# Kernel optimization log

Hardware: AMD Instinct MI355X
Metric: run time of the kernel (lower is better)

## Reference

```python
import jax, jax.numpy as jnp
import numpy as np

OUT_F, IN_F = 16384, 4096
TOKENS = 8192
PALETTE = 256


def setup_inputs() -> dict:
    key = jax.random.key(0)
    k1, k2, k3, k4 = jax.random.split(key, 4)
    input = jax.random.normal(k1, (TOKENS, IN_F), dtype=jnp.float32)
    weight_idx = jax.random.randint(k2, (OUT_F, IN_F), 0, PALETTE, dtype=jnp.int32)
    lookup_table = jax.random.normal(k3, (PALETTE,), dtype=jnp.float32)
    bias = jax.random.normal(k4, (OUT_F,), dtype=jnp.float32)
    return {"input": input, "weight_idx": weight_idx, "lookup_table": lookup_table, "bias": bias}


def reference(input, weight_idx, lookup_table, bias):
    # Dequantize: LUT gather expands uint8 indices to full-precision weights [out, in]
    full_weights = lookup_table[weight_idx]
    # F.linear: y = x @ W^T + b
    return jnp.einsum('ti,oi->to', input, full_weights) + bias
```

## Files before the change

### kernel.cpp

```cpp
#include <hip/hip_runtime.h>
#include <hip/hip_bf16.h>
#include <stdint.h>

#define TOKENS 8192
#define OUT_F  16384
#define IN_F   4096

typedef short bf16x8 __attribute__((ext_vector_type(8)));
typedef float f32x4  __attribute__((ext_vector_type(4)));

__device__ __forceinline__ unsigned short bf16_rne(float f) {
    union { float f; unsigned int u; } v; v.f = f;
    unsigned int u = v.u;
    u += 0x7fffu + ((u >> 16) & 1u);
    return (unsigned short)(u >> 16);
}

__device__ __forceinline__ unsigned int pack_bf16x2(float a, float b) {
    return (unsigned int)bf16_rne(a) | ((unsigned int)bf16_rne(b) << 16);
}

__device__ __forceinline__ void async_cp16(const void* gptr, void* ldsptr) {
    __builtin_amdgcn_global_load_lds(
        (const __attribute__((address_space(1))) unsigned int*)gptr,
        (__attribute__((address_space(3))) unsigned int*)ldsptr,
        16, 0, 0);
}

__global__ __launch_bounds__(256) void cvt_input_kernel(
    const float* __restrict__ in, unsigned short* __restrict__ out, int n8)
{
    int i = blockIdx.x * 256 + threadIdx.x;
    if (i >= n8) return;
    size_t base = (size_t)i * 8;
    float4 a = *(const float4*)(in + base);
    float4 b = *(const float4*)(in + base + 4);
    uint4 p;
    p.x = pack_bf16x2(a.x, a.y);  p.y = pack_bf16x2(a.z, a.w);
    p.z = pack_bf16x2(b.x, b.y);  p.w = pack_bf16x2(b.z, b.w);
    *(uint4*)(out + base) = p;
}

__global__ __launch_bounds__(256) void dequant_kernel(
    const int* __restrict__ idx, const float* __restrict__ lut,
    unsigned short* __restrict__ out, int n8)
{
    __shared__ float slut[256];
    slut[threadIdx.x] = lut[threadIdx.x];
    __syncthreads();
    int i = blockIdx.x * 256 + threadIdx.x;
    if (i >= n8) return;
    size_t base = (size_t)i * 8;
    int4 i0 = *(const int4*)(idx + base);
    int4 i1 = *(const int4*)(idx + base + 4);
    uint4 p;
    p.x = pack_bf16x2(slut[i0.x], slut[i0.y]);
    p.y = pack_bf16x2(slut[i0.z], slut[i0.w]);
    p.z = pack_bf16x2(slut[i1.x], slut[i1.y]);
    p.w = pack_bf16x2(slut[i1.z], slut[i1.w]);
    *(uint4*)(out + base) = p;
}

template<int MODE>
__global__ __launch_bounds__(256) void palett_gemm(
    const unsigned short* __restrict__ A,
    const unsigned short* __restrict__ B,
    const float* __restrict__ Af,
    const int* __restrict__ Widx,
    const float* __restrict__ lut,
    const float* __restrict__ bias,
    float* __restrict__ out)
{
    __shared__ __align__(16) unsigned short smA[128 * 32];
    __shared__ __align__(16) unsigned short smB[128 * 32];
    __shared__ float slut[256];

    const int t    = threadIdx.x;
    const int w    = t >> 6;
    const int l    = t & 63;
    const int quad = l >> 4;
    const int r16  = l & 15;
    const int wr   = w >> 1;
    const int wc   = w & 1;

    const int m0 = blockIdx.y * 128;
    const int n0 = blockIdx.x * 128;

    const int g0  = t * 8;
    const int row = g0 >> 5;
    const int col = g0 & 31;

    char* const smA_c = (char*)smA;
    char* const smB_c = (char*)smB;

    if constexpr (MODE == 1) {
        slut[t] = lut[t];
        __syncthreads();
    }

    uint32_t aoff[4], boff[4];
#pragma unroll
    for (int i = 0; i < 4; ++i) {
        aoff[i] = (uint32_t)(((wr * 64 + i * 16 + r16) * 32 + quad * 8) * 2);
        boff[i] = (uint32_t)(((wc * 64 + i * 16 + r16) * 32 + quad * 8) * 2);
    }

    f32x4 acc[4][4] = {};

    const unsigned short* a0 = nullptr; const unsigned short* a1 = nullptr;
    const unsigned short* b0 = nullptr; const unsigned short* b1 = nullptr;
    const float* af0 = nullptr; const float* af1 = nullptr;
    const int* wi0 = nullptr;   const int* wi1 = nullptr;
    if constexpr (MODE == 0) {
        a0 = A + (size_t)(m0 + row) * IN_F + col;
        a1 = A + (size_t)(m0 + row + 64) * IN_F + col;
        b0 = B + (size_t)(n0 + row) * IN_F + col;
        b1 = B + (size_t)(n0 + row + 64) * IN_F + col;
    } else {
        af0 = Af + (size_t)(m0 + row) * IN_F + col;
        af1 = Af + (size_t)(m0 + row + 64) * IN_F + col;
        wi0 = Widx + (size_t)(n0 + row) * IN_F + col;
        wi1 = Widx + (size_t)(n0 + row + 64) * IN_F + col;
    }

    const uint32_t ldsw0 = (uint32_t)(w * 1024);
    const uint32_t ldsw1 = (uint32_t)(4096 + w * 1024);

    for (int k0 = 0; k0 < IN_F; k0 += 32) {
        if constexpr (MODE == 0) {
            async_cp16(a0 + k0, smA_c + ldsw0);
            async_cp16(a1 + k0, smA_c + ldsw1);
            async_cp16(b0 + k0, smB_c + ldsw0);
            async_cp16(b1 + k0, smB_c + ldsw1);
        } else {
            float4 x0 = *(const float4*)(af0 + k0);
            float4 x1 = *(const float4*)(af0 + k0 + 4);
            uint4 p;
            p.x = pack_bf16x2(x0.x, x0.y); p.y = pack_bf16x2(x0.z, x0.w);
            p.z = pack_bf16x2(x1.x, x1.y); p.w = pack_bf16x2(x1.z, x1.w);
            *(uint4*)(smA_c + t * 16) = p;
            x0 = *(const float4*)(af1 + k0);
            x1 = *(const float4*)(af1 + k0 + 4);
            p.x = pack_bf16x2(x0.x, x0.y); p.y = pack_bf16x2(x0.z, x0.w);
            p.z = pack_bf16x2(x1.x, x1.y); p.w = pack_bf16x2(x1.z, x1.w);
            *(uint4*)(smA_c + 4096 + t * 16) = p;

            int4 j0 = *(const int4*)(wi0 + k0);
            int4 j1 = *(const int4*)(wi0 + k0 + 4);
            p.x = pack_bf16x2(slut[j0.x], slut[j0.y]);
            p.y = pack_bf16x2(slut[j0.z], slut[j0.w]);
            p.z = pack_bf16x2(slut[j1.x], slut[j1.y]);
            p.w = pack_bf16x2(slut[j1.z], slut[j1.w]);
            *(uint4*)(smB_c + t * 16) = p;
            j0 = *(const int4*)(wi1 + k0);
            j1 = *(const int4*)(wi1 + k0 + 4);
            p.x = pack_bf16x2(slut[j0.x], slut[j0.y]);
            p.y = pack_bf16x2(slut[j0.z], slut[j0.w]);
            p.z = pack_bf16x2(slut[j1.x], slut[j1.y]);
            p.w = pack_bf16x2(slut[j1.z], slut[j1.w]);
            *(uint4*)(smB_c + 4096 + t * 16) = p;
        }
        __syncthreads();

        bf16x8 afr[4], bfr[4];
#pragma unroll
        for (int i = 0; i < 4; ++i) afr[i] = *(const bf16x8*)(smA_c + aoff[i]);
#pragma unroll
        for (int j = 0; j < 4; ++j) bfr[j] = *(const bf16x8*)(smB_c + boff[j]);
#pragma unroll
        for (int i = 0; i < 4; ++i)
#pragma unroll
            for (int j = 0; j < 4; ++j)
                acc[i][j] = __builtin_amdgcn_mfma_f32_16x16x32_bf16(
                    afr[i], bfr[j], acc[i][j], 0, 0, 0);
        __syncthreads();
    }

    float bj[4];
#pragma unroll
    for (int j = 0; j < 4; ++j) bj[j] = bias[n0 + wc * 64 + j * 16 + r16];

#pragma unroll
    for (int i = 0; i < 4; ++i) {
        const int mbase = m0 + wr * 64 + i * 16 + quad * 4;
#pragma unroll
        for (int j = 0; j < 4; ++j) {
            const int n = n0 + wc * 64 + j * 16 + r16;
#pragma unroll
            for (int v = 0; v < 4; ++v) {
                out[(size_t)(mbase + v) * OUT_F + n] = acc[i][j][v] + bj[j];
            }
        }
    }
}

extern "C" void kernel_launch(void* const* d_in, const int* in_sizes, int n_in,
                              void* d_out, int out_size, void* d_ws, size_t ws_size,
                              hipStream_t stream) {
    const float* input = (const float*)d_in[0];
    const int*   widx  = (const int*)d_in[1];
    const float* lut   = (const float*)d_in[2];
    const float* bias  = (const float*)d_in[3];
    float* out = (float*)d_out;

    const size_t aBytes = (size_t)TOKENS * IN_F * sizeof(unsigned short);
    const size_t bBytes = (size_t)OUT_F  * IN_F * sizeof(unsigned short);

    dim3 grid(OUT_F / 128, TOKENS / 128);

    if (ws_size >= aBytes + bBytes) {
        unsigned short* wsA = (unsigned short*)d_ws;
        unsigned short* wsB = (unsigned short*)((char*)d_ws + aBytes);
        const int nA8 = (TOKENS * IN_F) / 8;
        const int nB8 = (OUT_F  * IN_F) / 8;
        cvt_input_kernel<<<(nA8 + 255) / 256, 256, 0, stream>>>(input, wsA, nA8);
        dequant_kernel<<<(nB8 + 255) / 256, 256, 0, stream>>>(widx, lut, wsB, nB8);
        palett_gemm<0><<<grid, 256, 0, stream>>>(wsA, wsB, nullptr, nullptr, lut, bias, out);
    } else {
        palett_gemm<1><<<grid, 256, 0, stream>>>(nullptr, nullptr, input, widx, lut, bias, out);
    }
}
```

Baseline: 1.948 ms.

## Replace bf16 GEMM with 256x256 double-buffered, swizzled, interleaved-stage kernel

Replaces the 128x128 single-buffered workspace GEMM with a 512-thread, 256x256-tile kernel. It double-buffers 64-wide K tiles in 128KB of LDS and interleaves async global-to-LDS loads with MFMA quarters under explicit barriers and vmcnt waits. It also XOR-swizzles the LDS columns to avoid bank conflicts, remaps block IDs for L2 locality, and raises wave priority around the MFMAs. The goal is to raise MFMA utilisation by hiding load latency and increasing data reuse per tile. In exchange it brings heavy register pressure and fragile hand-scheduled synchronisation.

```diff
diff --git a/kernel.cpp b/kernel.cpp
--- a/kernel.cpp
+++ b/kernel.cpp
@@ -1,5 +1,4 @@
 #include <hip/hip_runtime.h>
-#include <hip/hip_bf16.h>
 #include <stdint.h>
 
 #define TOKENS 8192
@@ -61,10 +60,154 @@
     *(uint4*)(out + base) = p;
 }
 
-template<int MODE>
-__global__ __launch_bounds__(256) void palett_gemm(
+__global__ __launch_bounds__(512, 2) void palett_gemm256(
     const unsigned short* __restrict__ A,
     const unsigned short* __restrict__ B,
+    const float* __restrict__ bias,
+    float* __restrict__ out)
+{
+    __shared__ __align__(16) char sm[131072];
+
+    const int t    = threadIdx.x;
+    const int w    = t >> 6;
+    const int l    = t & 63;
+    const int quad = l >> 4;
+    const int r16  = l & 15;
+    const int wr   = w >> 2;
+    const int wc   = w & 3;
+
+    const int orig = blockIdx.y * gridDim.x + blockIdx.x;
+    const int swzb = (orig & 7) * 256 + (orig >> 3);
+    const int n0   = (swzb & 63) << 8;
+    const int m0   = (swzb >> 6) << 8;
+
+    const int srow = w * 16 + (l >> 3);
+    const int scol = ((l & 7) ^ (l >> 3)) << 3;
+    const unsigned short* pA = A + (size_t)(m0 + srow) * IN_F + scol;
+    const unsigned short* pB = B + (size_t)(n0 + srow) * IN_F + scol;
+
+    const int cswz  = (r16 & 7) << 4;
+    const int col0  = (quad * 16) ^ cswz;
+    const int col1  = (64 + quad * 16) ^ cswz;
+    const int arow  = r16 * 128;
+    const int abase = wr * 16384;
+    const int bbase = 32768 + (wc >> 1) * 16384 + (wc & 1) * 8192;
+
+    f32x4  acc[8][4] = {};
+    bf16x8 rA[4][2], rB0[2][2], rB1[2][2];
+
+#define BARRIER() asm volatile("s_barrier" ::: "memory")
+
+#define STAGE(P, HOFF, LOFF, KOFF) do {                                          \
+    async_cp16((P) + (size_t)(HOFF) * IN_F + (KOFF), sm + (LOFF) + w * 2048);    \
+    async_cp16((P) + (size_t)((HOFF) + 8) * IN_F + (KOFF),                       \
+               sm + (LOFF) + w * 2048 + 1024);                                   \
+} while (0)
+
+#define READ_A(RB_, MH) do {                                                     \
+    _Pragma("unroll")                                                            \
+    for (int i_ = 0; i_ < 4; ++i_) {                                             \
+        rA[i_][0] = *(const bf16x8*)(sm + (RB_) + abase + ((MH)*4 + i_)*2048 + arow + col0); \
+        rA[i_][1] = *(const bf16x8*)(sm + (RB_) + abase + ((MH)*4 + i_)*2048 + arow + col1); \
+    }                                                                            \
+} while (0)
+
+#define READ_B(DST, RB_, NH) do {                                                \
+    _Pragma("unroll")                                                            \
+    for (int j_ = 0; j_ < 2; ++j_) {                                             \
+        DST[j_][0] = *(const bf16x8*)(sm + (RB_) + bbase + ((NH)*2 + j_)*2048 + arow + col0); \
+        DST[j_][1] = *(const bf16x8*)(sm + (RB_) + bbase + ((NH)*2 + j_)*2048 + arow + col1); \
+    }                                                                            \
+} while (0)
+
+#define MFMA_Q(MH, NH, RB) do {                                                  \
+    _Pragma("unroll")                                                            \
+    for (int i_ = 0; i_ < 4; ++i_) {                                             \
+        _Pragma("unroll")                                                        \
+        for (int j_ = 0; j_ < 2; ++j_) {                                         \
+            acc[(MH)*4+i_][(NH)*2+j_] = __builtin_amdgcn_mfma_f32_16x16x32_bf16( \
+                rA[i_][0], RB[j_][0], acc[(MH)*4+i_][(NH)*2+j_], 0, 0, 0);       \
+            acc[(MH)*4+i_][(NH)*2+j_] = __builtin_amdgcn_mfma_f32_16x16x32_bf16( \
+                rA[i_][1], RB[j_][1], acc[(MH)*4+i_][(NH)*2+j_], 0, 0, 0);       \
+        }                                                                        \
+    }                                                                            \
+} while (0)
+
+#define TILE(RB_, WB_, KOFF) do {                                                \
+                                                \
+    STAGE(pA, 0, (WB_) + 0, KOFF);                                               \
+    asm volatile("s_waitcnt vmcnt(2)" ::: "memory");                             \
+    BARRIER();                                                                   \
+    READ_A(RB_, 0);                                                              \
+    READ_B(rB0, RB_, 0);                                                         \
+    __builtin_amdgcn_s_setprio(1);                                               \
+    MFMA_Q(0, 0, rB0);                                                           \
+    __builtin_amdgcn_s_setprio(0);                                               \
+    READ_B(rB1, RB_, 1);                                                         \
+    BARRIER();                                                                   \
+                            \
+    STAGE(pA, 128, (WB_) + 16384, KOFF);                                         \
+    BARRIER();                                                                   \
+    __builtin_amdgcn_s_setprio(1);                                               \
+    MFMA_Q(0, 1, rB1);                                                           \
+    __builtin_amdgcn_s_setprio(0);                                               \
+    READ_A(RB_, 1);                                                              \
+    BARRIER();                                                                   \
+                                                                    \
+    STAGE(pB, 0, (WB_) + 32768, KOFF);                                           \
+    BARRIER();                                                                   \
+    __builtin_amdgcn_s_setprio(1);                                               \
+    MFMA_Q(1, 0, rB0);                                                           \
+    __builtin_amdgcn_s_setprio(0);                                               \
+    BARRIER();                                                                   \
+                                                                    \
+    STAGE(pB, 128, (WB_) + 49152, KOFF);                                         \
+    BARRIER();                                                                   \
+    __builtin_amdgcn_s_setprio(1);                                               \
+    MFMA_Q(1, 1, rB1);                                                           \
+    __builtin_amdgcn_s_setprio(0);                                               \
+    BARRIER();                                                                   \
+} while (0)
+
+    STAGE(pA, 0,   0,     0);
+    STAGE(pA, 128, 16384, 0);
+    STAGE(pB, 0,   32768, 0);
+    STAGE(pB, 128, 49152, 0);
+
+#pragma unroll 1
+    for (int it = 0; it < 32; ++it) {
+        const int k1 = (2 * it + 1) * 64;
+        const int k2 = ((2 * it + 2) & 63) * 64;
+        TILE(0,     65536, k1);
+        TILE(65536, 0,     k2);
+    }
+    asm volatile("s_waitcnt vmcnt(0)" ::: "memory");
+
+#undef TILE
+#undef MFMA_Q
+#undef READ_B
+#undef READ_A
+#undef STAGE
+#undef BARRIER
+
+    float bj[4];
+#pragma unroll
+    for (int j = 0; j < 4; ++j) bj[j] = bias[n0 + wc * 64 + j * 16 + r16];
+
+#pragma unroll
+    for (int mf = 0; mf < 8; ++mf) {
+        const int mrow = m0 + wr * 128 + mf * 16 + quad * 4;
+#pragma unroll
+        for (int nf = 0; nf < 4; ++nf) {
+            const int n = n0 + wc * 64 + nf * 16 + r16;
+#pragma unroll
+            for (int v = 0; v < 4; ++v)
+                out[(size_t)(mrow + v) * OUT_F + n] = acc[mf][nf][v] + bj[nf];
+        }
+    }
+}
+
+__global__ __launch_bounds__(256) void palett_gemm_fused(
     const float* __restrict__ Af,
     const int* __restrict__ Widx,
     const float* __restrict__ lut,
@@ -93,10 +236,8 @@
     char* const smA_c = (char*)smA;
     char* const smB_c = (char*)smB;
 
-    if constexpr (MODE == 1) {
-        slut[t] = lut[t];
-        __syncthreads();
-    }
+    slut[t] = lut[t];
+    __syncthreads();
 
     uint32_t aoff[4], boff[4];
 #pragma unroll
@@ -107,59 +248,38 @@
 
     f32x4 acc[4][4] = {};
 
-    const unsigned short* a0 = nullptr; const unsigned short* a1 = nullptr;
-    const unsigned short* b0 = nullptr; const unsigned short* b1 = nullptr;
-    const float* af0 = nullptr; const float* af1 = nullptr;
-    const int* wi0 = nullptr;   const int* wi1 = nullptr;
-    if constexpr (MODE == 0) {
-        a0 = A + (size_t)(m0 + row) * IN_F + col;
-        a1 = A + (size_t)(m0 + row + 64) * IN_F + col;
-        b0 = B + (size_t)(n0 + row) * IN_F + col;
-        b1 = B + (size_t)(n0 + row + 64) * IN_F + col;
-    } else {
-        af0 = Af + (size_t)(m0 + row) * IN_F + col;
-        af1 = Af + (size_t)(m0 + row + 64) * IN_F + col;
-        wi0 = Widx + (size_t)(n0 + row) * IN_F + col;
-        wi1 = Widx + (size_t)(n0 + row + 64) * IN_F + col;
-    }
-
-    const uint32_t ldsw0 = (uint32_t)(w * 1024);
-    const uint32_t ldsw1 = (uint32_t)(4096 + w * 1024);
+    const float* af0 = Af + (size_t)(m0 + row) * IN_F + col;
+    const float* af1 = Af + (size_t)(m0 + row + 64) * IN_F + col;
+    const int*   wi0 = Widx + (size_t)(n0 + row) * IN_F + col;
+    const int*   wi1 = Widx + (size_t)(n0 + row + 64) * IN_F + col;
 
     for (int k0 = 0; k0 < IN_F; k0 += 32) {
-        if constexpr (MODE == 0) {
-            async_cp16(a0 + k0, smA_c + ldsw0);
-            async_cp16(a1 + k0, smA_c + ldsw1);
-            async_cp16(b0 + k0, smB_c + ldsw0);
-            async_cp16(b1 + k0, smB_c + ldsw1);
-        } else {
-            float4 x0 = *(const float4*)(af0 + k0);
-            float4 x1 = *(const float4*)(af0 + k0 + 4);
-            uint4 p;
-            p.x = pack_bf16x2(x0.x, x0.y); p.y = pack_bf16x2(x0.z, x0.w);
-            p.z = pack_bf16x2(x1.x, x1.y); p.w = pack_bf16x2(x1.z, x1.w);
-            *(uint4*)(smA_c + t * 16) = p;
-            x0 = *(const float4*)(af1 + k0);
-            x1 = *(const float4*)(af1 + k0 + 4);
-            p.x = pack_bf16x2(x0.x, x0.y); p.y = pack_bf16x2(x0.z, x0.w);
-            p.z = pack_bf16x2(x1.x, x1.y); p.w = pack_bf16x2(x1.z, x1.w);
-            *(uint4*)(smA_c + 4096 + t * 16) = p;
-
-            int4 j0 = *(const int4*)(wi0 + k0);
-            int4 j1 = *(const int4*)(wi0 + k0 + 4);
-            p.x = pack_bf16x2(slut[j0.x], slut[j0.y]);
-            p.y = pack_bf16x2(slut[j0.z], slut[j0.w]);
-            p.z = pack_bf16x2(slut[j1.x], slut[j1.y]);
-            p.w = pack_bf16x2(slut[j1.z], slut[j1.w]);
-            *(uint4*)(smB_c + t * 16) = p;
-            j0 = *(const int4*)(wi1 + k0);
-            j1 = *(const int4*)(wi1 + k0 + 4);
-            p.x = pack_bf16x2(slut[j0.x], slut[j0.y]);
-            p.y = pack_bf16x2(slut[j0.z], slut[j0.w]);
-            p.z = pack_bf16x2(slut[j1.x], slut[j1.y]);
-            p.w = pack_bf16x2(slut[j1.z], slut[j1.w]);
-            *(uint4*)(smB_c + 4096 + t * 16) = p;
-        }
+        float4 x0 = *(const float4*)(af0 + k0);
+        float4 x1 = *(const float4*)(af0 + k0 + 4);
+        uint4 p;
+        p.x = pack_bf16x2(x0.x, x0.y); p.y = pack_bf16x2(x0.z, x0.w);
+        p.z = pack_bf16x2(x1.x, x1.y); p.w = pack_bf16x2(x1.z, x1.w);
+        *(uint4*)(smA_c + t * 16) = p;
+        x0 = *(const float4*)(af1 + k0);
+        x1 = *(const float4*)(af1 + k0 + 4);
+        p.x = pack_bf16x2(x0.x, x0.y); p.y = pack_bf16x2(x0.z, x0.w);
+        p.z = pack_bf16x2(x1.x, x1.y); p.w = pack_bf16x2(x1.z, x1.w);
+        *(uint4*)(smA_c + 4096 + t * 16) = p;
+
+        int4 j0 = *(const int4*)(wi0 + k0);
+        int4 j1 = *(const int4*)(wi0 + k0 + 4);
+        p.x = pack_bf16x2(slut[j0.x], slut[j0.y]);
+        p.y = pack_bf16x2(slut[j0.z], slut[j0.w]);
+        p.z = pack_bf16x2(slut[j1.x], slut[j1.y]);
+        p.w = pack_bf16x2(slut[j1.z], slut[j1.w]);
+        *(uint4*)(smB_c + t * 16) = p;
+        j0 = *(const int4*)(wi1 + k0);
+        j1 = *(const int4*)(wi1 + k0 + 4);
+        p.x = pack_bf16x2(slut[j0.x], slut[j0.y]);
+        p.y = pack_bf16x2(slut[j0.z], slut[j0.w]);
+        p.z = pack_bf16x2(slut[j1.x], slut[j1.y]);
+        p.w = pack_bf16x2(slut[j1.z], slut[j1.w]);
+        *(uint4*)(smB_c + 4096 + t * 16) = p;
         __syncthreads();
 
         bf16x8 afr[4], bfr[4];
@@ -206,8 +326,6 @@
     const size_t aBytes = (size_t)TOKENS * IN_F * sizeof(unsigned short);
     const size_t bBytes = (size_t)OUT_F  * IN_F * sizeof(unsigned short);
 
-    dim3 grid(OUT_F / 128, TOKENS / 128);
-
     if (ws_size >= aBytes + bBytes) {
         unsigned short* wsA = (unsigned short*)d_ws;
         unsigned short* wsB = (unsigned short*)((char*)d_ws + aBytes);
@@ -215,8 +333,10 @@
         const int nB8 = (OUT_F  * IN_F) / 8;
         cvt_input_kernel<<<(nA8 + 255) / 256, 256, 0, stream>>>(input, wsA, nA8);
         dequant_kernel<<<(nB8 + 255) / 256, 256, 0, stream>>>(widx, lut, wsB, nB8);
-        palett_gemm<0><<<grid, 256, 0, stream>>>(wsA, wsB, nullptr, nullptr, lut, bias, out);
+        dim3 grid2(OUT_F / 256, TOKENS / 256);
+        palett_gemm256<<<grid2, 512, 0, stream>>>(wsA, wsB, bias, out);
     } else {
-        palett_gemm<1><<<grid, 256, 0, stream>>>(nullptr, nullptr, input, widx, lut, bias, out);
-    }
-}
+        dim3 grid(OUT_F / 128, TOKENS / 128);
+        palett_gemm_fused<<<grid, 256, 0, stream>>>(input, widx, lut, bias, out);
+    }
+}
```

New measurement: 1.642 ms. 15.7% less time.
